# Kernel tuning notes

Measured on AMD Instinct MI355X. Metric: run time of the kernel, lower is better.

## Reference

```python
import jax, jax.numpy as jnp
import numpy as np

B, N, M, D = 64, 512, 1024, 128

def setup_inputs() -> dict:
    key = jax.random.key(0)
    ks = jax.random.split(key, 7)
    s = 1.0 / np.sqrt(D)
    return {
        "h_c": jax.random.normal(ks[0], (B, N, D), dtype=jnp.float32),
        "h_p": jax.random.normal(ks[1], (B, M, D), dtype=jnp.float32),
        "U_w": jax.random.normal(ks[2], (D, D), dtype=jnp.float32) * s,
        "U_b": jax.random.normal(ks[3], (D,), dtype=jnp.float32) * s,
        "V_w": jax.random.normal(ks[4], (D, D), dtype=jnp.float32) * s,
        "V_b": jax.random.normal(ks[5], (D,), dtype=jnp.float32) * s,
        "q": jax.random.normal(ks[6], (D,), dtype=jnp.float32),
    }

def reference(h_c, h_p, U_w, U_b, V_w, V_b, q):
    # ReLU-activated linear projections (torch Linear: x @ W.T + b)
    Uc = jax.nn.relu(jnp.einsum('bnd,ed->bne', h_c, U_w) + U_b)  # (B,N,D)
    Vp = jax.nn.relu(jnp.einsum('bmd,ed->bme', h_p, V_w) + V_b)  # (B,M,D)
    # bilinear attention scores and softmax over protein axis
    attn = jnp.einsum('bnd,bmd->bnm', Uc, Vp)                    # (B,N,M)
    weights = jax.nn.softmax(attn, axis=-1)
    context = jnp.einsum('bnm,bmd->bnd', weights, Vp)            # (B,N,D)
    joint = (Uc + context) * q                                   # (B,N,D)
    return joint.mean(axis=1)                                    # (B,D)
```

## Files before the change

### kernel.cpp

```cpp
#include <hip/hip_runtime.h>
#include <hip/hip_bf16.h>
#include <cstdint>

#define BB 64
#define NN 512
#define MM 1024
#define DD 128

typedef __bf16 bf16x8 __attribute__((ext_vector_type(8)));
typedef float f32x4 __attribute__((ext_vector_type(4)));

static __device__ __forceinline__ unsigned short f2bf(float f) {
    union { float f; unsigned int i; } v; v.f = f;
    unsigned int x = v.i;
    x += 0x7FFFu + ((x >> 16) & 1u);
    return (unsigned short)(x >> 16);
}
static __device__ __forceinline__ unsigned int f2bf2(float a, float b) {
    union { __hip_bfloat162 h; unsigned int u; } c;
    c.h = __float22bfloat162_rn(make_float2(a, b));
    return c.u;
}
static __device__ __forceinline__ void async16(const void* g, void* l) {
    __builtin_amdgcn_global_load_lds(
        (const __attribute__((address_space(1))) void*)g,
        (__attribute__((address_space(3))) void*)l, 16, 0, 0);
}

__global__ __launch_bounds__(256, 4) void proj_kernel(
    const float* __restrict__ hp,
    const float* __restrict__ hc,
    const float* __restrict__ Wu,
    const float* __restrict__ Wv,
    const float* __restrict__ Ub,
    const float* __restrict__ Vb,
    unsigned short* __restrict__ Y,
    unsigned short* __restrict__ YT,
    unsigned short* __restrict__ Ucg,
    float* __restrict__ colsum)
{
    __shared__ __align__(16) unsigned short Ws[128 * 136];
    unsigned short* Ys = Ws;
    unsigned short* Ts = Ws + 8192;
    const int t = threadIdx.x;
    const int lane = t & 63;
    const int wave = t >> 6;
    const int n16 = lane & 15, q = lane >> 4;
    const bool isC = blockIdx.x >= (BB * MM / 64);
    const float ws = isC ? 1.44269504088896f : 1.0f;

    const long row0 = isC ? (long)(blockIdx.x - BB * MM / 64) * 64
                          : (long)blockIdx.x * 64;
    const float* X = isC ? hc : hp;
    const float* Wf = isC ? Wu : Wv;
    const float* bias = isC ? Ub : Vb;

    float4 xv[8];
    {
        const float* xrow = X + (row0 + wave * 16 + n16) * DD + q * 8;
        #pragma unroll
        for (int kk = 0; kk < 4; ++kk) {
            xv[2 * kk]     = *(const float4*)(xrow + kk * 32);
            xv[2 * kk + 1] = *(const float4*)(xrow + kk * 32 + 4);
        }
    }
    {
        const float4* Wg = (const float4*)Wf;
        #pragma unroll
        for (int i = 0; i < 16; ++i) {
            int idx = i * 256 + t;
            float4 v = Wg[idx];
            int off = idx * 4;
            uint2 u = { f2bf2(v.x * ws, v.y * ws), f2bf2(v.z * ws, v.w * ws) };
            *(uint2*)&Ws[(off >> 7) * 136 + (off & 127)] = u;
        }
    }
    __syncthreads();

    f32x4 acc[8];
    #pragma unroll
    for (int j = 0; j < 8; ++j) acc[j] = {0.f, 0.f, 0.f, 0.f};

    #pragma unroll
    for (int kk = 0; kk < 4; ++kk) {
        float4 x0 = xv[2 * kk], x1 = xv[2 * kk + 1];
        union { bf16x8 v; unsigned int u[4]; } a;
        a.u[0] = f2bf2(x0.x, x0.y); a.u[1] = f2bf2(x0.z, x0.w);
        a.u[2] = f2bf2(x1.x, x1.y); a.u[3] = f2bf2(x1.z, x1.w);
        #pragma unroll
        for (int j = 0; j < 8; ++j) {
            bf16x8 b = *(const bf16x8*)&Ws[(j * 16 + n16) * 136 + q * 8 + kk * 32];
            acc[j] = __builtin_amdgcn_mfma_f32_16x16x32_bf16(a.v, b, acc[j], 0, 0, 0);
        }
    }

    unsigned short yb[8][4];
    float colp[8];
    #pragma unroll
    for (int j = 0; j < 8; ++j) {
        const float bv = bias[j * 16 + n16] * ws;
        float y[4], s = 0.f;
        #pragma unroll
        for (int r = 0; r < 4; ++r) {
            float v = acc[j][r] + bv;
            v = v > 0.f ? v : 0.f;
            y[r] = v;
            s += v;
        }
        colp[j] = s;
        uint2 u = { f2bf2(y[0], y[1]), f2bf2(y[2], y[3]) };
        *(uint2*)&yb[j][0] = u;
    }
    __syncthreads();

    if (!isC) {
        #pragma unroll
        for (int j = 0; j < 8; ++j) {
            const int e = j * 16 + n16;
            #pragma unroll
            for (int r = 0; r < 4; ++r)
                Ys[(wave * 16 + q * 4 + r) * 128 + e] = yb[j][r];
            *(uint2*)&Ts[e * 72 + wave * 16 + q * 4] = *(uint2*)&yb[j][0];
        }
        __syncthreads();
        uint4* dstY = (uint4*)(Y + row0 * DD);
        const long b = row0 >> 10;
        const long mt = (row0 & 1023) >> 6;
        uint4* dstT = (uint4*)(YT + ((b * 16 + mt) * 128) * 64);
        #pragma unroll
        for (int i = 0; i < 4; ++i) {
            int idx = i * 256 + t;
            dstY[idx] = ((const uint4*)Ys)[idx];
            int e = idx >> 3, m = (idx & 7) * 8;
            dstT[idx] = *(const uint4*)&Ts[e * 72 + m];
        }
    } else {
        #pragma unroll
        for (int j = 0; j < 8; ++j) {
            colp[j] += __shfl_xor(colp[j], 16);
            colp[j] += __shfl_xor(colp[j], 32);
        }
        float* cs = (float*)Ts;
        if (q == 0) {
            #pragma unroll
            for (int j = 0; j < 8; ++j)
                cs[wave * 128 + j * 16 + n16] = colp[j];
        }
        #pragma unroll
        for (int j = 0; j < 8; ++j) {
            const int e = j * 16 + n16;
            #pragma unroll
            for (int r = 0; r < 4; ++r)
                Ys[(wave * 16 + q * 4 + r) * 128 + e] = yb[j][r];
        }
        __syncthreads();
        const int c = (int)(row0 >> 6);
        uint4* dstU = (uint4*)(Ucg + row0 * DD);
        #pragma unroll
        for (int i = 0; i < 4; ++i) {
            int idx = i * 256 + t;
            dstU[idx] = ((const uint4*)Ys)[idx];
        }
        if (t < 128)
            colsum[(long)c * DD + t] = cs[t] + cs[128 + t] + cs[256 + t] + cs[384 + t];
    }
}

static __device__ __forceinline__ void attn_iter(
    int mt, unsigned short* bD, const unsigned short* bR,
    unsigned short* PsW, const unsigned short* PsR,
    const unsigned short* __restrict__ vpb,
    const unsigned short* __restrict__ vtb,
    int wave, int lane, int n16, int q, int a_off,
    const bf16x8 (&Bg)[4][4],
    bf16x8 (&aC)[4], bf16x8 (&aN)[4],
    f32x4 (&O)[8], float (&lpart)[4])
{
    const int nx = (mt + 2 > 15) ? 15 : mt + 2;
    {
        const unsigned short* st = vtb + nx * 8192;
        unsigned short* dst = bD + wave * 2048;
        #pragma unroll
        for (int i = 0; i < 4; ++i) {
            int L = wave * 256 + i * 64 + lane;
            int r = L >> 3, sc = L & 7, c = sc ^ (r & 7);
            async16(st + r * 64 + c * 8, dst + i * 512);
        }
    }
    __builtin_amdgcn_sched_barrier(0);
    {
        const unsigned short* pa = vpb + nx * 8192 + a_off;
        #pragma unroll
        for (int kk = 0; kk < 4; ++kk)
            aN[kk] = *(const bf16x8*)(pa + kk * 32);
    }
    asm volatile("s_waitcnt vmcnt(8)" ::: "memory");
    __builtin_amdgcn_sched_barrier(0);

    if (mt < 15) {
        f32x4 S[4];
        #pragma unroll
        for (int j = 0; j < 4; ++j) S[j] = {0.f, 0.f, 0.f, 0.f};
        __builtin_amdgcn_s_setprio(1);
        #pragma unroll
        for (int kk = 0; kk < 4; ++kk) {
            #pragma unroll
            for (int j = 0; j < 4; ++j)
                S[j] = __builtin_amdgcn_mfma_f32_16x16x32_bf16(aC[kk], Bg[j][kk], S[j], 0, 0, 0);
        }
        __builtin_amdgcn_s_setprio(0);
        #pragma unroll
        for (int j = 0; j < 4; ++j) {
            float p0 = __builtin_exp2f(S[j][0]);
            float p1 = __builtin_exp2f(S[j][1]);
            float p2 = __builtin_exp2f(S[j][2]);
            float p3 = __builtin_exp2f(S[j][3]);
            lpart[j] += (p0 + p1) + (p2 + p3);
            uint2 u = { f2bf2(p0, p1), f2bf2(p2, p3) };
            *(uint2*)&PsW[(j * 16 + n16) * 72 + wave * 16 + q * 4] = u;
        }
    }

    __builtin_amdgcn_s_setprio(1);
    #pragma unroll
    for (int kk = 0; kk < 2; ++kk) {
        bf16x8 a = *(const bf16x8*)&PsR[(wave * 16 + n16) * 72 + kk * 32 + q * 8];
        #pragma unroll
        for (int j = 0; j < 8; ++j) {
            bf16x8 bb = *(const bf16x8*)&bR[(j * 16 + n16) * 64 + ((kk * 4 + q) ^ (n16 & 7)) * 8];
            O[j] = __builtin_amdgcn_mfma_f32_16x16x32_bf16(a, bb, O[j], 0, 0, 0);
        }
    }
    __builtin_amdgcn_s_setprio(0);
    asm volatile("s_waitcnt lgkmcnt(0)" ::: "memory");
    __builtin_amdgcn_s_barrier();
    __builtin_amdgcn_sched_barrier(0);
}

__global__ __launch_bounds__(256, 2) void attn_kernel(
    const unsigned short* __restrict__ Ucg,
    const unsigned short* __restrict__ Vp,
    const unsigned short* __restrict__ VpT,
    float* __restrict__ part)
{
    __shared__ __align__(16) unsigned short smem[33792];
    unsigned short* Ps0 = smem + 24576;
    unsigned short* Ps1 = smem + 29184;

    const int t = threadIdx.x;
    const int lane = t & 63;
    const int wave = t >> 6;
    const int n16 = lane & 15, q = lane >> 4;

    const int id = blockIdx.x;
    const int xcd = id & 7;
    const int slot = id >> 3;
    const int b = xcd * 8 + (slot >> 3);
    const int nt = slot & 7;

    const unsigned short* vpb = Vp + (long)b * MM * DD;
    const unsigned short* vtb = VpT + (long)b * MM * DD;
    const unsigned short* ucb = Ucg + ((long)b * NN + nt * 64) * DD;

    bf16x8 Bg[4][4];
    #pragma unroll
    for (int j = 0; j < 4; ++j)
        #pragma unroll
        for (int kk = 0; kk < 4; ++kk)
            Bg[j][kk] = *(const bf16x8*)&ucb[(j * 16 + n16) * 128 + kk * 32 + q * 8];

    const int a_off = (wave * 16 + n16) * 128 + q * 8;
    bf16x8 aA[4], aB[4];
    #pragma unroll
    for (int kk = 0; kk < 4; ++kk)
        aA[kk] = *(const bf16x8*)&vpb[a_off + kk * 32];
    #pragma unroll
    for (int tt = 0; tt < 2; ++tt) {
        const unsigned short* st = vtb + tt * 8192;
        unsigned short* dst = smem + tt * 8192 + wave * 2048;
        #pragma unroll
        for (int i = 0; i < 4; ++i) {
            int L = wave * 256 + i * 64 + lane;
            int r = L >> 3, sc = L & 7, c = sc ^ (r & 7);
            async16(st + r * 64 + c * 8, dst + i * 512);
        }
    }
    #pragma unroll
    for (int kk = 0; kk < 4; ++kk)
        aB[kk] = *(const bf16x8*)&vpb[8192 + a_off + kk * 32];

    float lpart[4] = {0.f, 0.f, 0.f, 0.f};
    {
        f32x4 S[4];
        #pragma unroll
        for (int j = 0; j < 4; ++j) S[j] = {0.f, 0.f, 0.f, 0.f};
        #pragma unroll
        for (int kk = 0; kk < 4; ++kk) {
            #pragma unroll
            for (int j = 0; j < 4; ++j)
                S[j] = __builtin_amdgcn_mfma_f32_16x16x32_bf16(aA[kk], Bg[j][kk], S[j], 0, 0, 0);
        }
        #pragma unroll
        for (int j = 0; j < 4; ++j) {
            float p0 = __builtin_exp2f(S[j][0]);
            float p1 = __builtin_exp2f(S[j][1]);
            float p2 = __builtin_exp2f(S[j][2]);
            float p3 = __builtin_exp2f(S[j][3]);
            lpart[j] += (p0 + p1) + (p2 + p3);
            uint2 u = { f2bf2(p0, p1), f2bf2(p2, p3) };
            *(uint2*)&Ps0[(j * 16 + n16) * 72 + wave * 16 + q * 4] = u;
        }
    }
    asm volatile("s_waitcnt lgkmcnt(0)" ::: "memory");
    __builtin_amdgcn_s_barrier();
    __builtin_amdgcn_sched_barrier(0);

    f32x4 O[8];
    #pragma unroll
    for (int j = 0; j < 8; ++j) O[j] = {0.f, 0.f, 0.f, 0.f};

    unsigned short* b0 = smem;
    unsigned short* b1 = smem + 8192;
    unsigned short* b2 = smem + 16384;
    #pragma unroll 1
    for (int mt = 0; mt < 16; mt += 2) {
        attn_iter(mt,     b2, b0, Ps1, Ps0, vpb, vtb, wave, lane, n16, q, a_off, Bg, aB, aA, O, lpart);
        attn_iter(mt + 1, b0, b1, Ps0, Ps1, vpb, vtb, wave, lane, n16, q, a_off, Bg, aA, aB, O, lpart);
        unsigned short* tp = b0; b0 = b2; b2 = b1; b1 = tp;
    }

    #pragma unroll
    for (int j = 0; j < 4; ++j) {
        lpart[j] += __shfl_xor(lpart[j], 16);
        lpart[j] += __shfl_xor(lpart[j], 32);
    }
    float* lred = (float*)Ps0;
    float* red  = lred + 256;
    if (q == 0) {
        #pragma unroll
        for (int j = 0; j < 4; ++j)
            lred[wave * 64 + j * 16 + n16] = lpart[j];
    }
    __syncthreads();

    float inv[4];
    #pragma unroll
    for (int r = 0; r < 4; ++r) {
        int n = wave * 16 + q * 4 + r;
        inv[r] = 1.0f / (lred[n] + lred[64 + n] + lred[128 + n] + lred[192 + n]);
    }

    #pragma unroll
    for (int j = 0; j < 8; ++j) {
        float s = O[j][0] * inv[0] + O[j][1] * inv[1]
                + O[j][2] * inv[2] + O[j][3] * inv[3];
        s += __shfl_xor(s, 16);
        s += __shfl_xor(s, 32);
        if (q == 0)
            red[wave * 128 + j * 16 + n16] = s;
    }
    __syncthreads();
    if (t < 128) {
        float tot = red[t] + red[128 + t] + red[256 + t] + red[384 + t];
        part[(long)(b * 8 + nt) * DD + t] = tot;
    }
}

__global__ __launch_bounds__(256) void finalize_kernel(
    const float* __restrict__ part, const float* __restrict__ colsum,
    const float* __restrict__ qv, float* __restrict__ out)
{
    int i = blockIdx.x * 256 + threadIdx.x;
    int b = i >> 7, d = i & 127;
    const float* p  = part   + (long)b * 8 * DD + d;
    const float* cs = colsum + (long)b * 8 * DD + d;
    float s = 0.f, u = 0.f;
    #pragma unroll
    for (int nt = 0; nt < 8; ++nt) { s += p[nt * DD]; u += cs[nt * DD]; }
    out[i] = (s + u * 0.69314718055994531f) * qv[d] * (1.0f / (float)NN);
}

extern "C" void kernel_launch(void* const* d_in, const int* in_sizes, int n_in,
                              void* d_out, int out_size, void* d_ws, size_t ws_size,
                              hipStream_t stream) {
    const float* h_c = (const float*)d_in[0];
    const float* h_p = (const float*)d_in[1];
    const float* U_w = (const float*)d_in[2];
    const float* U_b = (const float*)d_in[3];
    const float* V_w = (const float*)d_in[4];
    const float* V_b = (const float*)d_in[5];
    const float* qv  = (const float*)d_in[6];
    float* out = (float*)d_out;

    unsigned short* Vp  = (unsigned short*)d_ws;
    unsigned short* VpT = Vp + (size_t)BB * MM * DD;
    unsigned short* Ucg = VpT + (size_t)BB * MM * DD;
    float* part   = (float*)(Ucg + (size_t)BB * NN * DD);
    float* colsum = part + (size_t)BB * 8 * DD;

    proj_kernel<<<BB * MM / 64 + BB * NN / 64, 256, 0, stream>>>(
        h_p, h_c, U_w, V_w, U_b, V_b, Vp, VpT, Ucg, colsum);
    attn_kernel<<<512, 256, 0, stream>>>(Ucg, Vp, VpT, part);
    finalize_kernel<<<32, 256, 0, stream>>>(part, colsum, qv, out);
}
```

Baseline: 139.0 us.

## Restructure attention kernel so each wave owns query rows and keeps P in registers

```diff
diff --git a/kernel.cpp b/kernel.cpp
--- a/kernel.cpp
+++ b/kernel.cpp
@@ -9,6 +9,7 @@
 
 typedef __bf16 bf16x8 __attribute__((ext_vector_type(8)));
 typedef float f32x4 __attribute__((ext_vector_type(4)));
+typedef short s16x4 __attribute__((ext_vector_type(4)));
 
 static __device__ __forceinline__ unsigned short f2bf(float f) {
     union { float f; unsigned int i; } v; v.f = f;
@@ -117,9 +118,12 @@
         #pragma unroll
         for (int j = 0; j < 8; ++j) {
             const int e = j * 16 + n16;
-            #pragma unroll
-            for (int r = 0; r < 4; ++r)
-                Ys[(wave * 16 + q * 4 + r) * 128 + e] = yb[j][r];
+            const int ehi = e >> 3, elo = e & 7;
+            #pragma unroll
+            for (int r = 0; r < 4; ++r) {
+                int row = wave * 16 + q * 4 + r;
+                Ys[row * 128 + ((ehi ^ (row & 7)) << 3) + elo] = yb[j][r];
+            }
             *(uint2*)&Ts[e * 72 + wave * 16 + q * 4] = *(uint2*)&yb[j][0];
         }
         __syncthreads();
@@ -164,77 +168,6 @@
         if (t < 128)
             colsum[(long)c * DD + t] = cs[t] + cs[128 + t] + cs[256 + t] + cs[384 + t];
     }
-}
-
-static __device__ __forceinline__ void attn_iter(
-    int mt, unsigned short* bD, const unsigned short* bR,
-    unsigned short* PsW, const unsigned short* PsR,
-    const unsigned short* __restrict__ vpb,
-    const unsigned short* __restrict__ vtb,
-    int wave, int lane, int n16, int q, int a_off,
-    const bf16x8 (&Bg)[4][4],
-    bf16x8 (&aC)[4], bf16x8 (&aN)[4],
-    f32x4 (&O)[8], float (&lpart)[4])
-{
-    const int nx = (mt + 2 > 15) ? 15 : mt + 2;
-    {
-        const unsigned short* st = vtb + nx * 8192;
-        unsigned short* dst = bD + wave * 2048;
-        #pragma unroll
-        for (int i = 0; i < 4; ++i) {
-            int L = wave * 256 + i * 64 + lane;
-            int r = L >> 3, sc = L & 7, c = sc ^ (r & 7);
-            async16(st + r * 64 + c * 8, dst + i * 512);
-        }
-    }
-    __builtin_amdgcn_sched_barrier(0);
-    {
-        const unsigned short* pa = vpb + nx * 8192 + a_off;
-        #pragma unroll
-        for (int kk = 0; kk < 4; ++kk)
-            aN[kk] = *(const bf16x8*)(pa + kk * 32);
-    }
-    asm volatile("s_waitcnt vmcnt(8)" ::: "memory");
-    __builtin_amdgcn_sched_barrier(0);
-
-    if (mt < 15) {
-        f32x4 S[4];
-        #pragma unroll
-        for (int j = 0; j < 4; ++j) S[j] = {0.f, 0.f, 0.f, 0.f};
-        __builtin_amdgcn_s_setprio(1);
-        #pragma unroll
-        for (int kk = 0; kk < 4; ++kk) {
-            #pragma unroll
-            for (int j = 0; j < 4; ++j)
-                S[j] = __builtin_amdgcn_mfma_f32_16x16x32_bf16(aC[kk], Bg[j][kk], S[j], 0, 0, 0);
-        }
-        __builtin_amdgcn_s_setprio(0);
-        #pragma unroll
-        for (int j = 0; j < 4; ++j) {
-            float p0 = __builtin_exp2f(S[j][0]);
-            float p1 = __builtin_exp2f(S[j][1]);
-            float p2 = __builtin_exp2f(S[j][2]);
-            float p3 = __builtin_exp2f(S[j][3]);
-            lpart[j] += (p0 + p1) + (p2 + p3);
-            uint2 u = { f2bf2(p0, p1), f2bf2(p2, p3) };
-            *(uint2*)&PsW[(j * 16 + n16) * 72 + wave * 16 + q * 4] = u;
-        }
-    }
-
-    __builtin_amdgcn_s_setprio(1);
-    #pragma unroll
-    for (int kk = 0; kk < 2; ++kk) {
-        bf16x8 a = *(const bf16x8*)&PsR[(wave * 16 + n16) * 72 + kk * 32 + q * 8];
-        #pragma unroll
-        for (int j = 0; j < 8; ++j) {
-            bf16x8 bb = *(const bf16x8*)&bR[(j * 16 + n16) * 64 + ((kk * 4 + q) ^ (n16 & 7)) * 8];
-            O[j] = __builtin_amdgcn_mfma_f32_16x16x32_bf16(a, bb, O[j], 0, 0, 0);
-        }
-    }
-    __builtin_amdgcn_s_setprio(0);
-    asm volatile("s_waitcnt lgkmcnt(0)" ::: "memory");
-    __builtin_amdgcn_s_barrier();
-    __builtin_amdgcn_sched_barrier(0);
 }
 
 __global__ __launch_bounds__(256, 2) void attn_kernel(
@@ -243,9 +176,7 @@
     const unsigned short* __restrict__ VpT,
     float* __restrict__ part)
 {
-    __shared__ __align__(16) unsigned short smem[33792];
-    unsigned short* Ps0 = smem + 24576;
-    unsigned short* Ps1 = smem + 29184;
+    __shared__ __align__(16) unsigned short smem[32768];
 
     const int t = threadIdx.x;
     const int lane = t & 63;
@@ -262,102 +193,120 @@
     const unsigned short* vtb = VpT + (long)b * MM * DD;
     const unsigned short* ucb = Ucg + ((long)b * NN + nt * 64) * DD;
 
-    bf16x8 Bg[4][4];
-    #pragma unroll
-    for (int j = 0; j < 4; ++j)
-        #pragma unroll
-        for (int kk = 0; kk < 4; ++kk)
-            Bg[j][kk] = *(const bf16x8*)&ucb[(j * 16 + n16) * 128 + kk * 32 + q * 8];
-
-    const int a_off = (wave * 16 + n16) * 128 + q * 8;
-    bf16x8 aA[4], aB[4];
+    bf16x8 Bn[4];
     #pragma unroll
     for (int kk = 0; kk < 4; ++kk)
-        aA[kk] = *(const bf16x8*)&vpb[a_off + kk * 32];
-    #pragma unroll
-    for (int tt = 0; tt < 2; ++tt) {
-        const unsigned short* st = vtb + tt * 8192;
-        unsigned short* dst = smem + tt * 8192 + wave * 2048;
+        Bn[kk] = *(const bf16x8*)&ucb[(wave * 16 + n16) * 128 + kk * 32 + q * 8];
+
+    {
+        #pragma unroll
+        for (int i = 0; i < 4; ++i) {
+            int L = wave * 256 + i * 64 + lane;
+            async16(vpb + L * 8, smem + wave * 2048 + i * 512);
+        }
         #pragma unroll
         for (int i = 0; i < 4; ++i) {
             int L = wave * 256 + i * 64 + lane;
             int r = L >> 3, sc = L & 7, c = sc ^ (r & 7);
-            async16(st + r * 64 + c * 8, dst + i * 512);
-        }
-    }
-    #pragma unroll
-    for (int kk = 0; kk < 4; ++kk)
-        aB[kk] = *(const bf16x8*)&vpb[8192 + a_off + kk * 32];
-
-    float lpart[4] = {0.f, 0.f, 0.f, 0.f};
-    {
+            async16(vtb + r * 64 + c * 8, smem + 16384 + wave * 2048 + i * 512);
+        }
+    }
+    asm volatile("s_waitcnt vmcnt(0) lgkmcnt(0)" ::: "memory");
+    __builtin_amdgcn_s_barrier();
+    __builtin_amdgcn_sched_barrier(0);
+
+    f32x4 O[8];
+    #pragma unroll
+    for (int j = 0; j < 8; ++j) O[j] = {0.f, 0.f, 0.f, 0.f};
+    float lsum = 0.f;
+
+    #pragma unroll 1
+    for (int mt = 0; mt < 16; ++mt) {
+        const unsigned short* V  = (mt & 1) ? smem + 8192  : smem;
+        const unsigned short* VT = (mt & 1) ? smem + 24576 : smem + 16384;
+        if (mt < 15) {
+            const unsigned short* sv = vpb + (mt + 1) * 8192;
+            const unsigned short* st = vtb + (mt + 1) * 8192;
+            unsigned short* dv = ((mt & 1) ? smem : smem + 8192) + wave * 2048;
+            unsigned short* dt = ((mt & 1) ? smem + 16384 : smem + 24576) + wave * 2048;
+            #pragma unroll
+            for (int i = 0; i < 4; ++i) {
+                int L = wave * 256 + i * 64 + lane;
+                async16(sv + L * 8, dv + i * 512);
+            }
+            #pragma unroll
+            for (int i = 0; i < 4; ++i) {
+                int L = wave * 256 + i * 64 + lane;
+                int r = L >> 3, sc = L & 7, c = sc ^ (r & 7);
+                async16(st + r * 64 + c * 8, dt + i * 512);
+            }
+        }
+        __builtin_amdgcn_sched_barrier(0);
+
         f32x4 S[4];
         #pragma unroll
         for (int j = 0; j < 4; ++j) S[j] = {0.f, 0.f, 0.f, 0.f};
-        #pragma unroll
-        for (int kk = 0; kk < 4; ++kk) {
-            #pragma unroll
-            for (int j = 0; j < 4; ++j)
-                S[j] = __builtin_amdgcn_mfma_f32_16x16x32_bf16(aA[kk], Bg[j][kk], S[j], 0, 0, 0);
-        }
+        __builtin_amdgcn_s_setprio(1);
+        #pragma unroll
+        for (int mtile = 0; mtile < 4; ++mtile) {
+            const int m = mtile * 16 + n16;
+            #pragma unroll
+            for (int kk = 0; kk < 4; ++kk) {
+                bf16x8 a = *(const bf16x8*)&V[m * 128 + (((kk * 4 + q) ^ (m & 7)) << 3)];
+                S[mtile] = __builtin_amdgcn_mfma_f32_16x16x32_bf16(a, Bn[kk], S[mtile], 0, 0, 0);
+            }
+        }
+        __builtin_amdgcn_s_setprio(0);
+
+        s16x4 av[4];
         #pragma unroll
         for (int j = 0; j < 4; ++j) {
             float p0 = __builtin_exp2f(S[j][0]);
             float p1 = __builtin_exp2f(S[j][1]);
             float p2 = __builtin_exp2f(S[j][2]);
             float p3 = __builtin_exp2f(S[j][3]);
-            lpart[j] += (p0 + p1) + (p2 + p3);
-            uint2 u = { f2bf2(p0, p1), f2bf2(p2, p3) };
-            *(uint2*)&Ps0[(j * 16 + n16) * 72 + wave * 16 + q * 4] = u;
-        }
-    }
-    asm volatile("s_waitcnt lgkmcnt(0)" ::: "memory");
-    __builtin_amdgcn_s_barrier();
-    __builtin_amdgcn_sched_barrier(0);
-
-    f32x4 O[8];
-    #pragma unroll
-    for (int j = 0; j < 8; ++j) O[j] = {0.f, 0.f, 0.f, 0.f};
-
-    unsigned short* b0 = smem;
-    unsigned short* b1 = smem + 8192;
-    unsigned short* b2 = smem + 16384;
-    #pragma unroll 1
-    for (int mt = 0; mt < 16; mt += 2) {
-        attn_iter(mt,     b2, b0, Ps1, Ps0, vpb, vtb, wave, lane, n16, q, a_off, Bg, aB, aA, O, lpart);
-        attn_iter(mt + 1, b0, b1, Ps0, Ps1, vpb, vtb, wave, lane, n16, q, a_off, Bg, aA, aB, O, lpart);
-        unsigned short* tp = b0; b0 = b2; b2 = b1; b1 = tp;
-    }
-
-    #pragma unroll
-    for (int j = 0; j < 4; ++j) {
-        lpart[j] += __shfl_xor(lpart[j], 16);
-        lpart[j] += __shfl_xor(lpart[j], 32);
-    }
-    float* lred = (float*)Ps0;
-    float* red  = lred + 256;
-    if (q == 0) {
-        #pragma unroll
-        for (int j = 0; j < 4; ++j)
-            lred[wave * 64 + j * 16 + n16] = lpart[j];
-    }
-    __syncthreads();
-
-    float inv[4];
-    #pragma unroll
-    for (int r = 0; r < 4; ++r) {
-        int n = wave * 16 + q * 4 + r;
-        inv[r] = 1.0f / (lred[n] + lred[64 + n] + lred[128 + n] + lred[192 + n]);
-    }
-
-    #pragma unroll
-    for (int j = 0; j < 8; ++j) {
-        float s = O[j][0] * inv[0] + O[j][1] * inv[1]
-                + O[j][2] * inv[2] + O[j][3] * inv[3];
+            lsum += (p0 + p1) + (p2 + p3);
+            union { unsigned int u[2]; s16x4 v; } pk;
+            pk.u[0] = f2bf2(p0, p1); pk.u[1] = f2bf2(p2, p3);
+            av[j] = pk.v;
+        }
+
+        __builtin_amdgcn_s_setprio(1);
+        #pragma unroll
+        for (int mtile = 0; mtile < 4; ++mtile) {
+            #pragma unroll
+            for (int dj = 0; dj < 8; ++dj) {
+                const int d = dj * 16 + n16;
+                s16x4 bv = *(const s16x4*)&VT[d * 64
+                    + (((mtile * 2 + (q >> 1)) ^ (d & 7)) << 3) + ((q & 1) << 2)];
+                O[dj] = __builtin_amdgcn_mfma_f32_16x16x16bf16_1k(av[mtile], bv, O[dj], 0, 0, 0);
+            }
+        }
+        __builtin_amdgcn_s_setprio(0);
+
+        asm volatile("s_waitcnt vmcnt(0) lgkmcnt(0)" ::: "memory");
+        __builtin_amdgcn_s_barrier();
+        __builtin_amdgcn_sched_barrier(0);
+    }
+
+    lsum += __shfl_xor(lsum, 16);
+    lsum += __shfl_xor(lsum, 32);
+    float* scr  = (float*)smem;
+    float* invw = scr + wave * 16;
+    if (lane < 16) invw[n16] = 1.0f / lsum;
+    float iv[4];
+    #pragma unroll
+    for (int r = 0; r < 4; ++r) iv[r] = invw[q * 4 + r];
+
+    float* red = scr + 64;
+    #pragma unroll
+    for (int dj = 0; dj < 8; ++dj) {
+        float s = O[dj][0] * iv[0] + O[dj][1] * iv[1]
+                + O[dj][2] * iv[2] + O[dj][3] * iv[3];
         s += __shfl_xor(s, 16);
         s += __shfl_xor(s, 32);
         if (q == 0)
-            red[wave * 128 + j * 16 + n16] = s;
+            red[wave * 128 + dj * 16 + n16] = s;
     }
     __syncthreads();
     if (t < 128) {
```

Measured after the change: 136.2 us. 2.0% less time.
